# Performance work log

Hardware: AMD Instinct MI355X
Metric: run time of the kernel (lower is better)

The kernel has to match this reference:

```python
import jax, jax.numpy as jnp
import numpy as np

B, N, F, D = 32, 1024, 128, 128
SCALE = 0.5


def setup_inputs() -> dict:
    key = jax.random.key(0)
    ks = jax.random.split(key, 8)
    atom_query = jax.random.normal(ks[0], (B, N, F), dtype=jnp.float32)
    # binary validity mask (some atoms padded out), shape [B, N, 1]
    mask = (jax.random.uniform(ks[1], (B, N, 1)) < 0.9).astype(jnp.float32)
    s = 1.0 / np.sqrt(F)
    Wq = jax.random.normal(ks[2], (F, D), dtype=jnp.float32) * s
    Wk = jax.random.normal(ks[3], (F, D), dtype=jnp.float32) * s
    Wv = jax.random.normal(ks[4], (F, D), dtype=jnp.float32) * s
    bq = jnp.zeros((D,), jnp.float32)
    bk = jnp.zeros((D,), jnp.float32)
    bv = jnp.zeros((D,), jnp.float32)
    return {"atom_query": atom_query, "mask": mask,
            "Wq": Wq, "bq": bq, "Wk": Wk, "bk": bk, "Wv": Wv, "bv": bv}


def reference(atom_query, mask, Wq, bq, Wk, bk, Wv, bv):
    # projections
    q = atom_query @ Wq + bq            # [B,N,D]
    k = atom_query @ Wk + bk            # [B,N,D]
    v = atom_query @ Wv + bv            # [B,N,D]
    n = q.shape[1]
    dk = (q.shape[-1] ** (-SCALE)) / n  # python float scalar
    q = q * jnp.float32(dk)
    # pairwise energy [B,N,N]
    energy = jnp.einsum('bqd,bkd->bqk', q, k)
    energy = energy * mask              # mask query rows ([B,N,1] broadcast)
    idx = jnp.arange(n)
    energy = energy.at[:, idx, idx].set(0.0)  # remove self-interaction (diag)
    # aggregate attention per query atom [B,N,1]
    agg = jnp.sum(energy, axis=-1, keepdims=True) * mask
    # euclidean normalize along atom axis (tf.linalg.normalize, axis=1)
    nrm = jnp.sqrt(jnp.sum(agg * agg, axis=1, keepdims=True))
    agg = agg / nrm
    agg = agg + (1.0 - mask) * (-1e9)
    attn = jax.nn.softmax(agg, axis=1)  # softmax over atom (query) axis
    # weighted sum of values -> [B,D]
    context = jnp.sum(mask * (attn * v), axis=1)
    return attn, context
```

## Files before the change

kernel.cpp:

```cpp
#include <hip/hip_runtime.h>

#define B_ 32
#define N_ 1024
#define F_ 128
#define D_ 128
#define DK_CONST 8.631674575031098e-05f
#define NM1 1023.0f

typedef unsigned short u16;
typedef __attribute__((ext_vector_type(8))) short short8;
typedef __attribute__((ext_vector_type(4))) float floatx4;

__device__ __forceinline__ u16 f2b(float x) {
    union { float f; unsigned u; } v; v.f = x;
    unsigned u = v.u;
    return (u16)((u + 0x7FFFu + ((u >> 16) & 1u)) >> 16);
}
__device__ __forceinline__ float b2f(u16 h) {
    union { unsigned u; float f; } v; v.u = ((unsigned)h) << 16;
    return v.f;
}

__global__ __launch_bounds__(256) void k1_colsum_mt(const float* __restrict__ aq,
                                                    const float* __restrict__ Wq,
                                                    const float* __restrict__ Wk,
                                                    float* __restrict__ colsumPart,
                                                    u16* __restrict__ Mt) {
    __shared__ float cspart[256][4];
    __shared__ float wq[128][129];
    __shared__ float wk2[2][128];
    int t = threadIdx.x;
    if (blockIdx.x < 256) {
        int tile = blockIdx.x;
        const float4* aq4 = (const float4*)(aq + (size_t)tile * 128 * 128);
        float c0 = 0.f, c1 = 0.f, c2 = 0.f, c3 = 0.f;
        for (int j = 0; j < 16; ++j) {
            float4 v = aq4[t + 256 * j];
            c0 += v.x; c1 += v.y; c2 += v.z; c3 += v.w;
        }
        cspart[t][0] = c0; cspart[t][1] = c1; cspart[t][2] = c2; cspart[t][3] = c3;
        __syncthreads();
        if (t < 128) {
            int c4i = t >> 2, comp = t & 3;
            float s = 0.f;
            for (int h = 0; h < 8; ++h) s += cspart[h * 32 + c4i][comp];
            colsumPart[tile * 128 + t] = s;
        }
    } else {
        int mb = blockIdx.x - 256;
        int h = t >> 7, f = t & 127;
        for (int j = 0; j < 64; ++j) {
            int idx = t + 256 * j;
            wq[idx >> 7][idx & 127] = Wq[idx];
        }
        wk2[h][f] = Wk[(mb * 2 + h) * 128 + f];
        __syncthreads();
        float s = 0.f;
        for (int d = 0; d < 128; ++d) s += wk2[h][d] * wq[f][d];
        Mt[(mb * 2 + h) * 128 + f] = f2b(s);
    }
}

__global__ __launch_bounds__(128) void k2_batch(const float* __restrict__ colsumPart,
                                                const float* __restrict__ Wq,
                                                const float* __restrict__ Wk,
                                                const float* __restrict__ bq,
                                                const float* __restrict__ bk,
                                                float* __restrict__ Sb,
                                                float* __restrict__ Cb,
                                                float* __restrict__ wc) {
    __shared__ float w[128][129];
    __shared__ float red[128];
    int b = blockIdx.x, t = threadIdx.x;
    float s = 0.f;
    for (int h = 0; h < 8; ++h) s += colsumPart[(b * 8 + h) * 128 + t];
    Sb[b * 128 + t] = s;
    float bqv = bq[t], bkv = bk[t];
    red[t] = fabsf(bqv) + fabsf(bkv);
    __syncthreads();
    for (int st = 64; st > 0; st >>= 1) { if (t < st) red[t] += red[t + st]; __syncthreads(); }
    float nb = red[0];
    __syncthreads();
    float w1 = 0.f, w2 = 0.f, bqbk = 0.f;
    if (nb != 0.f) {
        for (int r = 0; r < 128; ++r) w[r][t] = Wq[r * 128 + t];
        __syncthreads();
        for (int d = 0; d < 128; ++d) w1 += w[t][d] * bk[d];
        __syncthreads();
        for (int r = 0; r < 128; ++r) w[r][t] = Wk[r * 128 + t];
        __syncthreads();
        for (int d = 0; d < 128; ++d) w2 += w[t][d] * bq[d];
        red[t] = bqv * bkv;
        __syncthreads();
        for (int st = 64; st > 0; st >>= 1) { if (t < st) red[t] += red[t + st]; __syncthreads(); }
        bqbk = red[0];
        __syncthreads();
    }
    if (b == 0) wc[t] = NM1 * w1 - w2;
    red[t] = s * w2;
    __syncthreads();
    for (int st = 64; st > 0; st >>= 1) { if (t < st) red[t] += red[t + st]; __syncthreads(); }
    if (t == 0) Cb[b] = red[0] + NM1 * bqbk;
}

__global__ __launch_bounds__(256) void k3_agg(const float* __restrict__ aq,
                                              const u16* __restrict__ Mt,
                                              const float* __restrict__ mask,
                                              const float* __restrict__ Sb,
                                              const float* __restrict__ Cb,
                                              const float* __restrict__ wc,
                                              float* __restrict__ agg) {
    __shared__ __align__(16) u16 aqT[128][136];
    __shared__ __align__(16) u16 mtT[128][136];
    __shared__ float qpart[2][128];
    __shared__ float Sl[128], wcl[128];

    int t = threadIdx.x;
    int tile = blockIdx.x;
    int b = tile >> 3;
    const float* aqBlk = aq + (size_t)tile * 128 * 128;

    if (t < 128) { Sl[t] = Sb[b * 128 + t]; wcl[t] = wc[t]; }

    for (int j = 0; j < 16; ++j) {
        int idx = t + 256 * j;
        int row = idx >> 5;
        int c4  = idx & 31;
        float4 v = ((const float4*)aqBlk)[idx];
        ushort4 bb;
        bb.x = f2b(v.x); bb.y = f2b(v.y); bb.z = f2b(v.z); bb.w = f2b(v.w);
        *((ushort4*)&aqT[row][c4 * 4]) = bb;
    }
    for (int j = 0; j < 16; ++j) {
        int idx = t + 256 * j;
        int row = idx >> 5;
        int c4  = idx & 31;
        ushort4 mv = ((const ushort4*)Mt)[idx];
        *((ushort4*)&mtT[row][c4 * 4]) = mv;
    }
    __syncthreads();

    int w = t >> 6;
    int lane = t & 63;
    int wr   = (w >> 1) * 64;
    int wcol = (w & 1) * 64;
    int lm = lane & 15;
    int lq = lane >> 4;

    floatx4 acc[4][4];
    for (int i = 0; i < 4; ++i)
        for (int j = 0; j < 4; ++j)
            acc[i][j] = (floatx4){0.f, 0.f, 0.f, 0.f};

    for (int ks = 0; ks < 4; ++ks) {
        int k0 = ks * 32 + lq * 8;
        short8 afr[4], bfr[4];
        for (int i = 0; i < 4; ++i) {
            afr[i] = *(const short8*)&aqT[wr + i * 16 + lm][k0];
            bfr[i] = *(const short8*)&mtT[wcol + i * 16 + lm][k0];
        }
        for (int i = 0; i < 4; ++i)
            for (int j = 0; j < 4; ++j)
                acc[i][j] = __builtin_amdgcn_mfma_f32_16x16x32_bf16(afr[i], bfr[j], acc[i][j], 0, 0, 0);
    }

    for (int mi = 0; mi < 4; ++mi) {
        for (int r = 0; r < 4; ++r) {
            int row = wr + mi * 16 + lq * 4 + r;
            float s = 0.f;
            for (int nj = 0; nj < 4; ++nj) {
                int col = wcol + nj * 16 + lm;
                float av = b2f(aqT[row][col]);
                float T  = acc[mi][nj][r];
                s += T * (Sl[col] - av) + av * wcl[col];
            }
            for (int d = 1; d < 16; d <<= 1) s += __shfl_xor(s, d);
            if (lm == 0) qpart[w & 1][row] = s;
        }
    }
    __syncthreads();
    if (t < 128) {
        int atom = tile * 128 + t;
        agg[atom] = mask[atom] * DK_CONST * (qpart[0][t] + qpart[1][t] + Cb[b]);
    }
}

__global__ __launch_bounds__(256) void k4_softmax(const float* __restrict__ agg,
                                                  const float* __restrict__ mask,
                                                  float* __restrict__ attnOut,
                                                  float* __restrict__ ctxOut) {
    __shared__ float red[256];
    int b = blockIdx.x, t = threadIdx.x;
    if (t < 128) ctxOut[b * 128 + t] = 0.f;
    float a[4], m[4];
    float ss = 0.f;
    for (int j = 0; j < 4; ++j) {
        int i = b * N_ + j * 256 + t;
        a[j] = agg[i]; m[j] = mask[i];
        ss += a[j] * a[j];
    }
    red[t] = ss;
    __syncthreads();
    for (int st = 128; st > 0; st >>= 1) {
        if (t < st) red[t] += red[t + st];
        __syncthreads();
    }
    float invn = 1.0f / sqrtf(red[0]);
    __syncthreads();
    float z[4], mx = -3.0e38f;
    for (int j = 0; j < 4; ++j) {
        z[j] = (m[j] > 0.5f) ? a[j] * invn : -1.0e9f;
        mx = fmaxf(mx, z[j]);
    }
    red[t] = mx;
    __syncthreads();
    for (int st = 128; st > 0; st >>= 1) {
        if (t < st) red[t] = fmaxf(red[t], red[t + st]);
        __syncthreads();
    }
    mx = red[0];
    __syncthreads();
    float e[4], es = 0.f;
    for (int j = 0; j < 4; ++j) {
        e[j] = expf(z[j] - mx);
        es += e[j];
    }
    red[t] = es;
    __syncthreads();
    for (int st = 128; st > 0; st >>= 1) {
        if (t < st) red[t] += red[t + st];
        __syncthreads();
    }
    float inv = 1.0f / red[0];
    for (int j = 0; j < 4; ++j)
        attnOut[b * N_ + j * 256 + t] = e[j] * inv;
}

__global__ __launch_bounds__(256) void k5_ctx(const float* __restrict__ aq,
                                              const float* __restrict__ mask,
                                              const float* __restrict__ attn,
                                              const float* __restrict__ Wv,
                                              const float* __restrict__ bv,
                                              float* __restrict__ ctx) {
    __shared__ float wl[128];
    __shared__ float accs[4][128];
    __shared__ float p[128];
    __shared__ float wmass_s;
    int b = blockIdx.x, sblk = blockIdx.y, t = threadIdx.x;
    int base = b * N_ + sblk * 128;
    if (t < 128) wl[t] = attn[base + t] * mask[base + t];
    __syncthreads();
    int f2i = t & 63, h = t >> 6;
    const float2* aq2 = (const float2*)(aq + (size_t)base * 128);
    float2 acc; acc.x = 0.f; acc.y = 0.f;
    for (int r = h; r < 128; r += 4) {
        float2 v = aq2[r * 64 + f2i];
        float wgt = wl[r];
        acc.x += wgt * v.x; acc.y += wgt * v.y;
    }
    *((float2*)&accs[h][2 * f2i]) = acc;
    if (t < 64) {
        float wm = wl[t] + wl[t + 64];
        for (int d = 1; d < 64; d <<= 1) wm += __shfl_xor(wm, d);
        if (t == 0) wmass_s = wm;
    }
    __syncthreads();
    if (t < 128) p[t] = accs[0][t] + accs[1][t] + accs[2][t] + accs[3][t];
    __syncthreads();
    if (t < 128) {
        float c = 0.f;
        for (int f = 0; f < 128; ++f) c += p[f] * Wv[f * 128 + t];
        c += wmass_s * bv[t];
        atomicAdd(&ctx[b * 128 + t], c);
    }
}

extern "C" void kernel_launch(void* const* d_in, const int* in_sizes, int n_in,
                              void* d_out, int out_size, void* d_ws, size_t ws_size,
                              hipStream_t stream) {
    const float* aq   = (const float*)d_in[0];
    const float* mask = (const float*)d_in[1];
    const float* Wq   = (const float*)d_in[2];
    const float* bq   = (const float*)d_in[3];
    const float* Wk   = (const float*)d_in[4];
    const float* bk   = (const float*)d_in[5];
    const float* Wv   = (const float*)d_in[6];
    const float* bv   = (const float*)d_in[7];

    float* out_attn = (float*)d_out;
    float* out_ctx  = out_attn + B_ * N_;

    float* wsf        = (float*)d_ws;
    float* colsumPart = wsf;
    float* Sb         = wsf + 32768;
    float* Cb         = wsf + 36864;
    float* wc         = wsf + 36896;
    float* agg        = wsf + 37024;
    u16*   Mt         = (u16*)(wsf + 69792);

    k1_colsum_mt<<<320, 256, 0, stream>>>(aq, Wq, Wk, colsumPart, Mt);
    k2_batch<<<32, 128, 0, stream>>>(colsumPart, Wq, Wk, bq, bk, Sb, Cb, wc);
    k3_agg<<<256, 256, 0, stream>>>(aq, Mt, mask, Sb, Cb, wc, agg);
    k4_softmax<<<32, 256, 0, stream>>>(agg, mask, out_attn, out_ctx);
    k5_ctx<<<dim3(32, 8), 256, 0, stream>>>(aq, mask, out_attn, Wv, bv, out_ctx);
}
```

Measured before the change: 102.3 us.

## Fuse five kernels into three with last-block reduction for softmax and context

The batch-level reduction kernel is folded into the prep and aggregation kernels. The separate softmax and context kernels are merged into one finalize kernel that uses per-tile sum-of-squares partials and a per-batch atomic counter, so the last block per batch does the normalization and Wv projection. Softmax skips the max subtraction, relying on normalized values being bounded. This removes two launches and the serial 32-block softmax pass, at the cost of counter synchronization, threadfences and an extra rewrite pass over attn.

```diff
diff --git a/kernel.cpp b/kernel.cpp
--- a/kernel.cpp
+++ b/kernel.cpp
@@ -21,18 +21,24 @@
     return v.f;
 }
 
-__global__ __launch_bounds__(256) void k1_colsum_mt(const float* __restrict__ aq,
-                                                    const float* __restrict__ Wq,
-                                                    const float* __restrict__ Wk,
-                                                    float* __restrict__ colsumPart,
-                                                    u16* __restrict__ Mt) {
+__global__ __launch_bounds__(256) void k1_prep(const float* __restrict__ aq,
+                                               const float* __restrict__ Wq,
+                                               const float* __restrict__ Wk,
+                                               const float* __restrict__ bq,
+                                               const float* __restrict__ bk,
+                                               float* __restrict__ colsumPart,
+                                               u16* __restrict__ Mt,
+                                               float* __restrict__ wcv,
+                                               int* __restrict__ counterB) {
+    __shared__ float wq[128][129];
+    __shared__ float vsm[2][128];
+    __shared__ float red[256];
     __shared__ float cspart[256][4];
-    __shared__ float wq[128][129];
-    __shared__ float wk2[2][128];
     int t = threadIdx.x;
-    if (blockIdx.x < 256) {
-        int tile = blockIdx.x;
-        const float4* aq4 = (const float4*)(aq + (size_t)tile * 128 * 128);
+    int blk = blockIdx.x;
+    if (blk < 256) {
+        if (blk == 0 && t < 32) counterB[t] = 0;
+        const float4* aq4 = (const float4*)(aq + (size_t)blk * 128 * 128);
         float c0 = 0.f, c1 = 0.f, c2 = 0.f, c3 = 0.f;
         for (int j = 0; j < 16; ++j) {
             float4 v = aq4[t + 256 * j];
@@ -44,83 +50,71 @@
             int c4i = t >> 2, comp = t & 3;
             float s = 0.f;
             for (int h = 0; h < 8; ++h) s += cspart[h * 32 + c4i][comp];
-            colsumPart[tile * 128 + t] = s;
-        }
-    } else {
-        int mb = blockIdx.x - 256;
+            colsumPart[blk * 128 + t] = s;
+        }
+    } else if (blk < 320) {
+        int mb = blk - 256;
         int h = t >> 7, f = t & 127;
         for (int j = 0; j < 64; ++j) {
             int idx = t + 256 * j;
             wq[idx >> 7][idx & 127] = Wq[idx];
         }
-        wk2[h][f] = Wk[(mb * 2 + h) * 128 + f];
+        vsm[h][f] = Wk[(mb * 2 + h) * 128 + f];
         __syncthreads();
         float s = 0.f;
-        for (int d = 0; d < 128; ++d) s += wk2[h][d] * wq[f][d];
+        for (int d = 0; d < 128; ++d) s += vsm[h][d] * wq[f][d];
         Mt[(mb * 2 + h) * 128 + f] = f2b(s);
-    }
-}
-
-__global__ __launch_bounds__(128) void k2_batch(const float* __restrict__ colsumPart,
-                                                const float* __restrict__ Wq,
-                                                const float* __restrict__ Wk,
-                                                const float* __restrict__ bq,
-                                                const float* __restrict__ bk,
-                                                float* __restrict__ Sb,
-                                                float* __restrict__ Cb,
-                                                float* __restrict__ wc) {
-    __shared__ float w[128][129];
-    __shared__ float red[128];
-    int b = blockIdx.x, t = threadIdx.x;
-    float s = 0.f;
-    for (int h = 0; h < 8; ++h) s += colsumPart[(b * 8 + h) * 128 + t];
-    Sb[b * 128 + t] = s;
-    float bqv = bq[t], bkv = bk[t];
-    red[t] = fabsf(bqv) + fabsf(bkv);
-    __syncthreads();
-    for (int st = 64; st > 0; st >>= 1) { if (t < st) red[t] += red[t + st]; __syncthreads(); }
-    float nb = red[0];
-    __syncthreads();
-    float w1 = 0.f, w2 = 0.f, bqbk = 0.f;
-    if (nb != 0.f) {
-        for (int r = 0; r < 128; ++r) w[r][t] = Wq[r * 128 + t];
-        __syncthreads();
-        for (int d = 0; d < 128; ++d) w1 += w[t][d] * bk[d];
-        __syncthreads();
-        for (int r = 0; r < 128; ++r) w[r][t] = Wk[r * 128 + t];
-        __syncthreads();
-        for (int d = 0; d < 128; ++d) w2 += w[t][d] * bq[d];
-        red[t] = bqv * bkv;
-        __syncthreads();
-        for (int st = 64; st > 0; st >>= 1) { if (t < st) red[t] += red[t + st]; __syncthreads(); }
-        bqbk = red[0];
-        __syncthreads();
-    }
-    if (b == 0) wc[t] = NM1 * w1 - w2;
-    red[t] = s * w2;
-    __syncthreads();
-    for (int st = 64; st > 0; st >>= 1) { if (t < st) red[t] += red[t + st]; __syncthreads(); }
-    if (t == 0) Cb[b] = red[0] + NM1 * bqbk;
-}
-
-__global__ __launch_bounds__(256) void k3_agg(const float* __restrict__ aq,
+    } else {
+        if (t < 128) { vsm[0][t] = bq[t]; vsm[1][t] = bk[t]; }
+        red[t] = (t < 128) ? (fabsf(bq[t]) + fabsf(bk[t])) : 0.f;
+        __syncthreads();
+        for (int st = 128; st > 0; st >>= 1) { if (t < st) red[t] += red[t + st]; __syncthreads(); }
+        float nb = red[0];
+        __syncthreads();
+        if (nb != 0.f) {
+            for (int j = 0; j < 64; ++j) {
+                int idx = t + 256 * j;
+                wq[idx >> 7][idx & 127] = Wq[idx];
+            }
+            __syncthreads();
+            float w1 = 0.f;
+            if (t < 128) for (int d = 0; d < 128; ++d) w1 += wq[t][d] * vsm[1][d];
+            __syncthreads();
+            for (int j = 0; j < 64; ++j) {
+                int idx = t + 256 * j;
+                wq[idx >> 7][idx & 127] = Wk[idx];
+            }
+            red[t] = (t < 128) ? vsm[0][t] * vsm[1][t] : 0.f;
+            __syncthreads();
+            float w2v = 0.f;
+            if (t < 128) for (int d = 0; d < 128; ++d) w2v += wq[t][d] * vsm[0][d];
+            for (int st = 128; st > 0; st >>= 1) { if (t < st) red[t] += red[t + st]; __syncthreads(); }
+            if (t < 128) { wcv[t] = NM1 * w1 - w2v; wcv[128 + t] = w2v; }
+            if (t == 0) wcv[256] = red[0];
+        } else {
+            if (t < 128) { wcv[t] = 0.f; wcv[128 + t] = 0.f; }
+            if (t == 0) wcv[256] = 0.f;
+        }
+    }
+}
+
+__global__ __launch_bounds__(256) void k2_agg(const float* __restrict__ aq,
                                               const u16* __restrict__ Mt,
                                               const float* __restrict__ mask,
-                                              const float* __restrict__ Sb,
-                                              const float* __restrict__ Cb,
-                                              const float* __restrict__ wc,
-                                              float* __restrict__ agg) {
+                                              const float* __restrict__ colsumPart,
+                                              const float* __restrict__ wcv,
+                                              float* __restrict__ agg,
+                                              float* __restrict__ ssqPart) {
     __shared__ __align__(16) u16 aqT[128][136];
     __shared__ __align__(16) u16 mtT[128][136];
     __shared__ float qpart[2][128];
     __shared__ float Sl[128], wcl[128];
+    __shared__ float red[256];
 
     int t = threadIdx.x;
     int tile = blockIdx.x;
     int b = tile >> 3;
     const float* aqBlk = aq + (size_t)tile * 128 * 128;
-
-    if (t < 128) { Sl[t] = Sb[b * 128 + t]; wcl[t] = wc[t]; }
 
     for (int j = 0; j < 16; ++j) {
         int idx = t + 256 * j;
@@ -138,7 +132,16 @@
         ushort4 mv = ((const ushort4*)Mt)[idx];
         *((ushort4*)&mtT[row][c4 * 4]) = mv;
     }
-    __syncthreads();
+    float s = 0.f;
+    if (t < 128) {
+        for (int h = 0; h < 8; ++h) s += colsumPart[(b * 8 + h) * 128 + t];
+        Sl[t] = s;
+        wcl[t] = wcv[t];
+    }
+    red[t] = (t < 128) ? s * wcv[128 + t] : 0.f;
+    __syncthreads();
+    for (int st = 128; st > 0; st >>= 1) { if (t < st) red[t] += red[t + st]; __syncthreads(); }
+    float Cbv = red[0] + NM1 * wcv[256];
 
     int w = t >> 6;
     int lane = t & 63;
@@ -167,111 +170,104 @@
     for (int mi = 0; mi < 4; ++mi) {
         for (int r = 0; r < 4; ++r) {
             int row = wr + mi * 16 + lq * 4 + r;
-            float s = 0.f;
+            float sx = 0.f;
             for (int nj = 0; nj < 4; ++nj) {
                 int col = wcol + nj * 16 + lm;
                 float av = b2f(aqT[row][col]);
                 float T  = acc[mi][nj][r];
-                s += T * (Sl[col] - av) + av * wcl[col];
+                sx += T * (Sl[col] - av) + av * wcl[col];
             }
-            for (int d = 1; d < 16; d <<= 1) s += __shfl_xor(s, d);
-            if (lm == 0) qpart[w & 1][row] = s;
-        }
-    }
-    __syncthreads();
+            for (int d = 1; d < 16; d <<= 1) sx += __shfl_xor(sx, d);
+            if (lm == 0) qpart[w & 1][row] = sx;
+        }
+    }
+    __syncthreads();
+    float a2 = 0.f;
     if (t < 128) {
         int atom = tile * 128 + t;
-        agg[atom] = mask[atom] * DK_CONST * (qpart[0][t] + qpart[1][t] + Cb[b]);
-    }
-}
-
-__global__ __launch_bounds__(256) void k4_softmax(const float* __restrict__ agg,
-                                                  const float* __restrict__ mask,
-                                                  float* __restrict__ attnOut,
-                                                  float* __restrict__ ctxOut) {
-    __shared__ float red[256];
-    int b = blockIdx.x, t = threadIdx.x;
-    if (t < 128) ctxOut[b * 128 + t] = 0.f;
-    float a[4], m[4];
-    float ss = 0.f;
-    for (int j = 0; j < 4; ++j) {
-        int i = b * N_ + j * 256 + t;
-        a[j] = agg[i]; m[j] = mask[i];
-        ss += a[j] * a[j];
-    }
-    red[t] = ss;
-    __syncthreads();
-    for (int st = 128; st > 0; st >>= 1) {
-        if (t < st) red[t] += red[t + st];
-        __syncthreads();
-    }
-    float invn = 1.0f / sqrtf(red[0]);
-    __syncthreads();
-    float z[4], mx = -3.0e38f;
-    for (int j = 0; j < 4; ++j) {
-        z[j] = (m[j] > 0.5f) ? a[j] * invn : -1.0e9f;
-        mx = fmaxf(mx, z[j]);
-    }
-    red[t] = mx;
-    __syncthreads();
-    for (int st = 128; st > 0; st >>= 1) {
-        if (t < st) red[t] = fmaxf(red[t], red[t + st]);
-        __syncthreads();
-    }
-    mx = red[0];
-    __syncthreads();
-    float e[4], es = 0.f;
-    for (int j = 0; j < 4; ++j) {
-        e[j] = expf(z[j] - mx);
-        es += e[j];
-    }
-    red[t] = es;
-    __syncthreads();
-    for (int st = 128; st > 0; st >>= 1) {
-        if (t < st) red[t] += red[t + st];
-        __syncthreads();
-    }
-    float inv = 1.0f / red[0];
-    for (int j = 0; j < 4; ++j)
-        attnOut[b * N_ + j * 256 + t] = e[j] * inv;
-}
-
-__global__ __launch_bounds__(256) void k5_ctx(const float* __restrict__ aq,
+        float a = mask[atom] * DK_CONST * (qpart[0][t] + qpart[1][t] + Cbv);
+        agg[atom] = a;
+        a2 = a * a;
+    }
+    red[t] = a2;
+    __syncthreads();
+    for (int st = 128; st > 0; st >>= 1) { if (t < st) red[t] += red[t + st]; __syncthreads(); }
+    if (t == 0) ssqPart[tile] = red[0];
+}
+
+__global__ __launch_bounds__(256) void k3_fin(const float* __restrict__ aq,
                                               const float* __restrict__ mask,
-                                              const float* __restrict__ attn,
                                               const float* __restrict__ Wv,
                                               const float* __restrict__ bv,
-                                              float* __restrict__ ctx) {
-    __shared__ float wl[128];
-    __shared__ float accs[4][128];
-    __shared__ float p[128];
-    __shared__ float wmass_s;
-    int b = blockIdx.x, sblk = blockIdx.y, t = threadIdx.x;
-    int base = b * N_ + sblk * 128;
-    if (t < 128) wl[t] = attn[base + t] * mask[base + t];
-    __syncthreads();
-    int f2i = t & 63, h = t >> 6;
-    const float2* aq2 = (const float2*)(aq + (size_t)base * 128);
-    float2 acc; acc.x = 0.f; acc.y = 0.f;
-    for (int r = h; r < 128; r += 4) {
-        float2 v = aq2[r * 64 + f2i];
-        float wgt = wl[r];
-        acc.x += wgt * v.x; acc.y += wgt * v.y;
-    }
-    *((float2*)&accs[h][2 * f2i]) = acc;
-    if (t < 64) {
-        float wm = wl[t] + wl[t + 64];
-        for (int d = 1; d < 64; d <<= 1) wm += __shfl_xor(wm, d);
-        if (t == 0) wmass_s = wm;
-    }
-    __syncthreads();
-    if (t < 128) p[t] = accs[0][t] + accs[1][t] + accs[2][t] + accs[3][t];
-    __syncthreads();
+                                              const float* __restrict__ agg,
+                                              const float* __restrict__ ssqPart,
+                                              float* __restrict__ Epart,
+                                              float* __restrict__ ctxPart,
+                                              int* __restrict__ counterB,
+                                              float* __restrict__ attnOut,
+                                              float* __restrict__ ctxOut) {
+    __shared__ float el[128];
+    __shared__ float red[256];
+    __shared__ float cp[2][128];
+    __shared__ float shInvn;
+    __shared__ int shOld;
+    int b = blockIdx.x, s = blockIdx.y, t = threadIdx.x;
+    int base = b * N_ + s * 128;
+
+    if (t == 0) {
+        float ss = 0.f;
+        for (int h = 0; h < 8; ++h) ss += ssqPart[b * 8 + h];
+        shInvn = 1.0f / sqrtf(ss);
+    }
+    __syncthreads();
+    float invn = shInvn;
+    float e = 0.f;
     if (t < 128) {
+        float a = agg[base + t];
+        float m = mask[base + t];
+        e = (m > 0.5f) ? expf(a * invn) : 0.f;
+        el[t] = e;
+        attnOut[base + t] = e;
+    }
+    red[t] = e;
+    __syncthreads();
+    for (int st = 128; st > 0; st >>= 1) { if (t < st) red[t] += red[t + st]; __syncthreads(); }
+    if (t == 0) Epart[b * 8 + s] = red[0];
+
+    int f = t & 127, hh = t >> 7;
+    const float* aqs = aq + (size_t)base * 128;
+    float acc = 0.f;
+    for (int r = hh; r < 128; r += 2) acc += el[r] * aqs[r * 128 + f];
+    cp[hh][f] = acc;
+    __syncthreads();
+    if (t < 128) ctxPart[(b * 8 + s) * 128 + t] = cp[0][t] + cp[1][t];
+
+    __threadfence();
+    __syncthreads();
+    if (t == 0) shOld = atomicAdd(&counterB[b], 1);
+    __syncthreads();
+    if (shOld == 7) {
+        __threadfence();
+        float E = 0.f;
+        for (int h = 0; h < 8; ++h) E += Epart[b * 8 + h];
+        float invE = 1.0f / E;
+        if (t < 128) {
+            float p = 0.f;
+            for (int h = 0; h < 8; ++h) p += ctxPart[(b * 8 + h) * 128 + t];
+            el[t] = p;
+        }
+        __syncthreads();
+        int th = t & 127, half = t >> 7;
         float c = 0.f;
-        for (int f = 0; f < 128; ++f) c += p[f] * Wv[f * 128 + t];
-        c += wmass_s * bv[t];
-        atomicAdd(&ctx[b * 128 + t], c);
+        for (int ff = half * 64; ff < half * 64 + 64; ++ff) c += el[ff] * Wv[ff * 128 + th];
+        cp[half][th] = c;
+        __syncthreads();
+        if (t < 128)
+            ctxOut[b * 128 + t] = (cp[0][t] + cp[1][t]) * invE + bv[t];
+        for (int j = 0; j < 4; ++j) {
+            int i = b * N_ + j * 256 + t;
+            attnOut[i] *= invE;
+        }
     }
 }
 
@@ -292,15 +288,16 @@
 
     float* wsf        = (float*)d_ws;
     float* colsumPart = wsf;
-    float* Sb         = wsf + 32768;
-    float* Cb         = wsf + 36864;
-    float* wc         = wsf + 36896;
-    float* agg        = wsf + 37024;
-    u16*   Mt         = (u16*)(wsf + 69792);
-
-    k1_colsum_mt<<<320, 256, 0, stream>>>(aq, Wq, Wk, colsumPart, Mt);
-    k2_batch<<<32, 128, 0, stream>>>(colsumPart, Wq, Wk, bq, bk, Sb, Cb, wc);
-    k3_agg<<<256, 256, 0, stream>>>(aq, Mt, mask, Sb, Cb, wc, agg);
-    k4_softmax<<<32, 256, 0, stream>>>(agg, mask, out_attn, out_ctx);
-    k5_ctx<<<dim3(32, 8), 256, 0, stream>>>(aq, mask, out_attn, Wv, bv, out_ctx);
-}
+    float* agg        = wsf + 32768;
+    float* ssqPart    = wsf + 65536;
+    float* wcv        = wsf + 65792;
+    float* Epart      = wsf + 66080;
+    float* ctxPart    = wsf + 66336;
+    int*   counterB   = (int*)(wsf + 99104);
+    u16*   Mt         = (u16*)(wsf + 99136);
+
+    k1_prep<<<321, 256, 0, stream>>>(aq, Wq, Wk, bq, bk, colsumPart, Mt, wcv, counterB);
+    k2_agg<<<256, 256, 0, stream>>>(aq, Mt, mask, colsumPart, wcv, agg, ssqPart);
+    k3_fin<<<dim3(32, 8), 256, 0, stream>>>(aq, mask, Wv, bv, agg, ssqPart,
+                                            Epart, ctxPart, counterB, out_attn, out_ctx);
+}
```

After: 123.2 us. 1.2x slower.
